# Performance work log

Measured on AMD Instinct MI355X. Metric: run time of the kernel, lower is better.

Reference implementation:

```python
import jax, jax.numpy as jnp
import numpy as np

N, M, D, H, T = 8192, 8192, 64, 32, 8
KERNEL_SCALE = 1.0


def setup_inputs() -> dict:
    key = jax.random.key(0)
    ks = jax.random.split(key, 8)
    s1 = 1.0 / np.sqrt(D)
    s2 = 1.0 / np.sqrt(H)
    return {
        "X": jax.random.normal(ks[0], (N, D), jnp.float32),
        "Y": jax.random.normal(ks[1], (M, D), jnp.float32),
        "Y_target": jax.random.normal(ks[2], (M, T), jnp.float32),
        "W1": jax.random.normal(ks[3], (D, H), jnp.float32) * s1,
        "b1": jnp.zeros((H,), jnp.float32),
        "W2": jax.random.normal(ks[4], (H, H), jnp.float32) * s2,
        "b2": jnp.zeros((H,), jnp.float32),
        "W3": jax.random.normal(ks[5], (H, H), jnp.float32) * s2,
        "b3": jnp.zeros((H,), jnp.float32),
    }


def _mlp(x, W1, b1, W2, b2, W3, b3):
    h = jax.nn.relu(x @ W1 + b1)
    h = jax.nn.relu(h @ W2 + b2)
    return jax.nn.relu(h @ W3 + b3)


def reference(X, Y, Y_target, W1, b1, W2, b2, W3, b3):
    Xf = _mlp(X, W1, b1, W2, b2, W3, b3)  # [N, H]
    Yf = _mlp(Y, W1, b1, W2, b2, W3, b3)  # [M, H]
    sq = (
        jnp.sum(Xf * Xf, axis=1, keepdims=True)
        + jnp.sum(Yf * Yf, axis=1)[None, :]
        - 2.0 * (Xf @ Yf.T)
    )
    sq = jnp.maximum(sq, 0.0)  # guard tiny negatives from cancellation
    kernel = jnp.exp(-sq / (2.0 * KERNEL_SCALE**2))  # [N, M]
    weights = kernel / jnp.sum(kernel, axis=1, keepdims=True)
    return weights @ Y_target  # [N, T]
```

## Files before the change

### kernel.cpp

```cpp
#include <hip/hip_runtime.h>
#include <hip/hip_bf16.h>
#include <cstddef>

#define N_ROWS 8192
#define M_ROWS 8192
#define D_IN   64
#define H_DIM  32
#define T_OUT  8
#define FDIM   48

#define NSPLIT   32
#define JSLICE   (M_ROWS / NSPLIT)
#define JTILE    32
#define NTILES   (JSLICE / JTILE)
#define LOG2E    1.4426950408889634f
#define NHALF_SC (-0.72134752044448169f)

#define KH_OFF 0
#define KL_OFF 3072
#define YH_OFF 6144
#define YL_OFF 8192
#define BUFSZ  10240

typedef _Float16 half8  __attribute__((ext_vector_type(8)));
typedef _Float16 half4v __attribute__((ext_vector_type(4)));
typedef __fp16   fp16x2 __attribute__((ext_vector_type(2)));
typedef float    f32x16 __attribute__((ext_vector_type(16)));

__device__ __forceinline__ half8 ld_h8(const _Float16* p) {
    return *(const half8*)p;
}


__global__ __launch_bounds__(256) void feat_kernel(
    const float* __restrict__ X, const float* __restrict__ Y,
    const float* __restrict__ W1, const float* __restrict__ b1,
    const float* __restrict__ W2, const float* __restrict__ b2,
    const float* __restrict__ W3, const float* __restrict__ b3,
    _Float16* __restrict__ fh, _Float16* __restrict__ fl)
{
    __shared__ float xs [32 * 65];
    __shared__ float w1l[64 * 36];
    __shared__ float w2l[32 * 36];
    __shared__ float w3l[32 * 36];
    __shared__ float h1t[32 * 33];
    __shared__ float h2t[32 * 33];
    __shared__ float psums[8 * 32];
    __shared__ float bl[96];

    const int tid = threadIdx.x;
    const int rowbase = blockIdx.x * 32;
    const bool isX = rowbase < N_ROWS;
    const float* src = isX ? (X + (size_t)rowbase * D_IN)
                           : (Y + (size_t)(rowbase - N_ROWS) * D_IN);

    {
        const float4* g4 = (const float4*)src;
        int i0 = tid * 2;
        float4 v0 = g4[i0], v1 = g4[i0 + 1];
        int f0 = tid * 8;
        int r = f0 >> 6, c = f0 & 63;
        float* dst = xs + r * 65 + c;
        dst[0] = v0.x; dst[1] = v0.y; dst[2] = v0.z; dst[3] = v0.w;
        dst[4] = v1.x; dst[5] = v1.y; dst[6] = v1.z; dst[7] = v1.w;
    }
    {
        const float4* g4 = (const float4*)W1;
        int i0 = tid * 2;
        float4 v0 = g4[i0], v1 = g4[i0 + 1];
        int f0 = tid * 8;
        int r = f0 >> 5, c = f0 & 31;
        float* dst = w1l + r * 36 + c;
        ((float4*)dst)[0] = v0; ((float4*)dst)[1] = v1;
    }
    {
        int f0 = tid * 4;
        int r = f0 >> 5, c = f0 & 31;
        *(float4*)(w2l + r * 36 + c) = ((const float4*)W2)[tid];
        *(float4*)(w3l + r * 36 + c) = ((const float4*)W3)[tid];
    }
    if (tid < 32) { bl[tid] = b1[tid]; bl[32 + tid] = b2[tid]; bl[64 + tid] = b3[tid]; }
    __syncthreads();

    const int r  = tid & 31;
    const int c0 = (tid >> 5) * 4;

    float4 a1 = *(const float4*)(bl + c0);
    #pragma unroll
    for (int k = 0; k < 64; ++k) {
        float xv = xs[r * 65 + k];
        float4 w = *(const float4*)(w1l + k * 36 + c0);
        a1.x = fmaf(xv, w.x, a1.x);
        a1.y = fmaf(xv, w.y, a1.y);
        a1.z = fmaf(xv, w.z, a1.z);
        a1.w = fmaf(xv, w.w, a1.w);
    }
    h1t[(c0 + 0) * 33 + r] = fmaxf(a1.x, 0.f);
    h1t[(c0 + 1) * 33 + r] = fmaxf(a1.y, 0.f);
    h1t[(c0 + 2) * 33 + r] = fmaxf(a1.z, 0.f);
    h1t[(c0 + 3) * 33 + r] = fmaxf(a1.w, 0.f);
    __syncthreads();

    float4 a2 = *(const float4*)(bl + 32 + c0);
    #pragma unroll
    for (int k = 0; k < 32; ++k) {
        float xv = h1t[k * 33 + r];
        float4 w = *(const float4*)(w2l + k * 36 + c0);
        a2.x = fmaf(xv, w.x, a2.x);
        a2.y = fmaf(xv, w.y, a2.y);
        a2.z = fmaf(xv, w.z, a2.z);
        a2.w = fmaf(xv, w.w, a2.w);
    }
    h2t[(c0 + 0) * 33 + r] = fmaxf(a2.x, 0.f);
    h2t[(c0 + 1) * 33 + r] = fmaxf(a2.y, 0.f);
    h2t[(c0 + 2) * 33 + r] = fmaxf(a2.z, 0.f);
    h2t[(c0 + 3) * 33 + r] = fmaxf(a2.w, 0.f);
    __syncthreads();

    float4 a3 = *(const float4*)(bl + 64 + c0);
    #pragma unroll
    for (int k = 0; k < 32; ++k) {
        float xv = h2t[k * 33 + r];
        float4 w = *(const float4*)(w3l + k * 36 + c0);
        a3.x = fmaf(xv, w.x, a3.x);
        a3.y = fmaf(xv, w.y, a3.y);
        a3.z = fmaf(xv, w.z, a3.z);
        a3.w = fmaf(xv, w.w, a3.w);
    }
    float v0 = fmaxf(a3.x, 0.f), v1 = fmaxf(a3.y, 0.f);
    float v2 = fmaxf(a3.z, 0.f), v3 = fmaxf(a3.w, 0.f);

    psums[(tid >> 5) * 32 + r] = v0 * v0 + v1 * v1 + v2 * v2 + v3 * v3;

    const float scale = isX ? LOG2E : 1.0f;
    union { _Float16 h[4]; uint2 u; } hh, ll;
    float sv0 = v0 * scale, sv1 = v1 * scale, sv2 = v2 * scale, sv3 = v3 * scale;
    hh.h[0] = (_Float16)sv0; hh.h[1] = (_Float16)sv1;
    hh.h[2] = (_Float16)sv2; hh.h[3] = (_Float16)sv3;
    ll.h[0] = (_Float16)(sv0 - (float)hh.h[0]);
    ll.h[1] = (_Float16)(sv1 - (float)hh.h[1]);
    ll.h[2] = (_Float16)(sv2 - (float)hh.h[2]);
    ll.h[3] = (_Float16)(sv3 - (float)hh.h[3]);
    {
        const int tile = blockIdx.x;
        const int ch = c0 >> 4, hb = (c0 >> 3) & 1, off = c0 & 7;
        const size_t fi = (((size_t)(tile * 3 + ch) * 64) + hb * 32 + r) * 8 + off;
        *(uint2*)(fh + fi) = hh.u;
        *(uint2*)(fl + fi) = ll.u;
    }

    __syncthreads();
    if (tid < 32) {
        float nrm = 0.f;
        #pragma unroll
        for (int g = 0; g < 8; ++g) nrm += psums[g * 32 + tid];
        float qn = NHALF_SC * nrm;
        float d32 = isX ? qn : 1.0f;
        float d33 = isX ? 1.0f : qn;
        union { _Float16 h[8]; uint4 q; } eh, el, ez;
        #pragma unroll
        for (int i = 0; i < 8; ++i) { eh.h[i] = (_Float16)0.f; el.h[i] = (_Float16)0.f; ez.h[i] = (_Float16)0.f; }
        _Float16 h32 = (_Float16)d32, h33 = (_Float16)d33;
        eh.h[0] = h32; eh.h[1] = h33;
        el.h[0] = (_Float16)(d32 - (float)h32);
        el.h[1] = (_Float16)(d33 - (float)h33);
        const int tile = blockIdx.x;
        const size_t f0 = (((size_t)(tile * 3 + 2) * 64) + tid) * 8;
        const size_t f1 = (((size_t)(tile * 3 + 2) * 64) + 32 + tid) * 8;
        *(uint4*)(fh + f0) = eh.q;  *(uint4*)(fh + f1) = ez.q;
        *(uint4*)(fl + f0) = el.q;  *(uint4*)(fl + f1) = ez.q;
    }
}

__global__ __launch_bounds__(256) void ytt_kernel(
    const float* __restrict__ Yt,
    _Float16* __restrict__ yfh, _Float16* __restrict__ yfl)
{
    const int idx = blockIdx.x * 256 + threadIdx.x;
    const int lane = idx & 63;
    const int jtg  = idx >> 6;
    const int g    = jtg & 3;
    const int jt   = jtg >> 2;
    const int t    = lane & 31;
    const int h    = lane >> 5;
    const int j    = jt * 32 + g * 8 + h * 4;
    union { _Float16 hh[4]; uint2 u; } H, L;
    #pragma unroll
    for (int i = 0; i < 4; ++i) {
        float v = (t < T_OUT) ? Yt[(size_t)(j + i) * T_OUT + t]
                              : (t == 8 ? 1.0f : 0.0f);
        _Float16 hi = (_Float16)v;
        H.hh[i] = hi;
        L.hh[i] = (_Float16)(v - (float)hi);
    }
    *(uint2*)(yfh + (size_t)idx * 4) = H.u;
    *(uint2*)(yfl + (size_t)idx * 4) = L.u;
}

__global__ __launch_bounds__(256, 4) void pair_kernel(
    const _Float16* __restrict__ fh, const _Float16* __restrict__ fl,
    const _Float16* __restrict__ yfh, const _Float16* __restrict__ yfl,
    float* __restrict__ pout, float* __restrict__ psum)
{
    __shared__ char smem[2 * BUFSZ];

    const int tid  = threadIdx.x;
    const int wave = tid >> 6;
    const int lane = tid & 63;
    const int n    = lane & 31;
    const int h    = lane >> 5;

    const int rowtile = blockIdx.x * 4 + wave;
    const int rowbase = rowtile * 32;
    const int s       = blockIdx.y;
    const int ktile0  = (N_ROWS / 32) + s * NTILES;

    const size_t qoff = (size_t)rowtile * 1536 + (size_t)lane * 8;
    half8 qh0 = ld_h8(fh + qoff);
    half8 qh1 = ld_h8(fh + qoff + 512);
    half8 qh2 = ld_h8(fh + qoff + 1024);
    half8 ql0 = ld_h8(fl + qoff);
    half8 ql1 = ld_h8(fl + qoff + 512);
    half8 ql2 = ld_h8(fl + qoff + 1024);

    auto prefetch = [&](int jt, char* buf) {
        const char* srcKh = (const char*)(fh + (size_t)(ktile0 + jt) * 1536);
        const char* srcKl = (const char*)(fl + (size_t)(ktile0 + jt) * 1536);
        const char* srcYh = (const char*)(yfh + (size_t)(s * NTILES + jt) * 1024);
        const char* srcYl = (const char*)(yfl + (size_t)(s * NTILES + jt) * 1024);
        #pragma unroll
        for (int r = 0; r < 3; ++r) {
            const int c0 = wave * 64 + r * 256;
            const int c  = c0 + lane;
            const char* g; char* l;
            if (c0 < 192)      { g = srcKh + (size_t)c * 16;         l = buf + KH_OFF + c * 16; }
            else if (c0 < 384) { g = srcKl + (size_t)(c - 192) * 16; l = buf + KL_OFF + (c - 192) * 16; }
            else if (c0 < 512) { g = srcYh + (size_t)(c - 384) * 16; l = buf + YH_OFF + (c - 384) * 16; }
            else if (c0 < 640) { g = srcYl + (size_t)(c - 512) * 16; l = buf + YL_OFF + (c - 512) * 16; }
            else break;
            __builtin_amdgcn_global_load_lds(
                (const __attribute__((address_space(1))) void*)g,
                (__attribute__((address_space(3))) void*)l, 16, 0, 0);
        }
    };

    f32x16 o = {};

    prefetch(0, smem);
    __syncthreads();

    for (int jt = 0; jt < NTILES; ++jt) {
        char* cur = smem + (jt & 1) * BUFSZ;
        if (jt + 1 < NTILES) prefetch(jt + 1, smem + ((jt + 1) & 1) * BUFSZ);

        half8 kh0 = *(const half8*)(cur + KH_OFF + lane * 16);
        half8 kh1 = *(const half8*)(cur + KH_OFF + 1024 + lane * 16);
        half8 kh2 = *(const half8*)(cur + KH_OFF + 2048 + lane * 16);
        half8 kl0 = *(const half8*)(cur + KL_OFF + lane * 16);
        half8 kl1 = *(const half8*)(cur + KL_OFF + 1024 + lane * 16);
        half8 kl2 = *(const half8*)(cur + KL_OFF + 2048 + lane * 16);

        f32x16 acc = {};
        acc = __builtin_amdgcn_mfma_f32_32x32x16_f16(kh0, qh0, acc, 0, 0, 0);
        acc = __builtin_amdgcn_mfma_f32_32x32x16_f16(kh1, qh1, acc, 0, 0, 0);
        acc = __builtin_amdgcn_mfma_f32_32x32x16_f16(kh2, qh2, acc, 0, 0, 0);
        acc = __builtin_amdgcn_mfma_f32_32x32x16_f16(kh0, ql0, acc, 0, 0, 0);
        acc = __builtin_amdgcn_mfma_f32_32x32x16_f16(kh1, ql1, acc, 0, 0, 0);
        acc = __builtin_amdgcn_mfma_f32_32x32x16_f16(kh2, ql2, acc, 0, 0, 0);
        acc = __builtin_amdgcn_mfma_f32_32x32x16_f16(kl0, qh0, acc, 0, 0, 0);
        acc = __builtin_amdgcn_mfma_f32_32x32x16_f16(kl1, qh1, acc, 0, 0, 0);
        acc = __builtin_amdgcn_mfma_f32_32x32x16_f16(kl2, qh2, acc, 0, 0, 0);

        half4v phi[4];
        #pragma unroll
        for (int g = 0; g < 4; ++g) {
            float w0 = __builtin_amdgcn_exp2f(fminf(acc[4*g+0], 0.f));
            float w1 = __builtin_amdgcn_exp2f(fminf(acc[4*g+1], 0.f));
            float w2 = __builtin_amdgcn_exp2f(fminf(acc[4*g+2], 0.f));
            float w3 = __builtin_amdgcn_exp2f(fminf(acc[4*g+3], 0.f));
            fp16x2 p01 = __builtin_amdgcn_cvt_pkrtz(w0, w1);
            fp16x2 p23 = __builtin_amdgcn_cvt_pkrtz(w2, w3);
            union { unsigned int u[2]; half4v v; } ph;
            ph.u[0] = __builtin_bit_cast(unsigned int, p01);
            ph.u[1] = __builtin_bit_cast(unsigned int, p23);
            phi[g] = ph.v;
        }

        #pragma unroll
        for (int g = 0; g < 4; ++g) {
            half4v bh = *(const half4v*)(cur + YH_OFF + (g * 64 + lane) * 8);
            half4v bv = *(const half4v*)(cur + YL_OFF + (g * 64 + lane) * 8);
            o = __builtin_amdgcn_mfma_f32_32x32x8f16(phi[g], bh, o, 0, 0, 0);
            o = __builtin_amdgcn_mfma_f32_32x32x8f16(phi[g], bv, o, 0, 0, 0);
        }

        __syncthreads();
    }

    const int t = n;
    if (t <= 8) {
        #pragma unroll
        for (int r = 0; r < 16; ++r) {
            int i = (r & 3) + 8 * (r >> 2) + 4 * h;
            int row = rowbase + i;
            float v = o[r];
            if (t < 8)
                pout[((size_t)s * N_ROWS + row) * T_OUT + t] = v;
            else
                psum[(size_t)s * N_ROWS + row] = v;
        }
    }
}

__global__ __launch_bounds__(256) void reduce_kernel(
    const float* __restrict__ pout, const float* __restrict__ psum,
    float* __restrict__ out)
{
    const int id = blockIdx.x * 256 + threadIdx.x;
    const int i = id >> 3;
    float sv = 0.f, sw = 0.f;
    #pragma unroll
    for (int s = 0; s < NSPLIT; ++s) {
        sv += pout[(size_t)s * N_ROWS * T_OUT + id];
        sw += psum[(size_t)s * N_ROWS + i];
    }
    out[id] = sv / sw;
}

extern "C" void kernel_launch(void* const* d_in, const int* in_sizes, int n_in,
                              void* d_out, int out_size, void* d_ws, size_t ws_size,
                              hipStream_t stream)
{
    const float* X  = (const float*)d_in[0];
    const float* Y  = (const float*)d_in[1];
    const float* Yt = (const float*)d_in[2];
    const float* W1 = (const float*)d_in[3];
    const float* b1 = (const float*)d_in[4];
    const float* W2 = (const float*)d_in[5];
    const float* b2 = (const float*)d_in[6];
    const float* W3 = (const float*)d_in[7];
    const float* b3 = (const float*)d_in[8];
    float* out = (float*)d_out;

    char* ws = (char*)d_ws;
    const size_t n_feat = (size_t)((N_ROWS + M_ROWS) / 32) * 3 * 512;
    _Float16* fh  = (_Float16*)ws;   ws += n_feat * 2;
    _Float16* fl  = (_Float16*)ws;   ws += n_feat * 2;
    const size_t n_yf = (size_t)(M_ROWS / JTILE) * 4 * 64 * 4;
    _Float16* yfh = (_Float16*)ws;   ws += n_yf * 2;
    _Float16* yfl = (_Float16*)ws;   ws += n_yf * 2;
    float*    pout = (float*)ws;     ws += (size_t)NSPLIT * N_ROWS * T_OUT * 4;
    float*    psum = (float*)ws;

    feat_kernel<<<(N_ROWS + M_ROWS) / 32, 256, 0, stream>>>(
        X, Y, W1, b1, W2, b2, W3, b3, fh, fl);
    ytt_kernel<<<(M_ROWS / JTILE) * 4 * 64 / 256, 256, 0, stream>>>(Yt, yfh, yfl);

    dim3 grid2(N_ROWS / 128, NSPLIT);
    pair_kernel<<<grid2, 256, 0, stream>>>(fh, fl, yfh, yfl, pout, psum);

    reduce_kernel<<<(N_ROWS * T_OUT) / 256, 256, 0, stream>>>(pout, psum, out);
}
```

Baseline: 112.6 us.

## Merge prep kernels and process two j-tiles per barrier stage

Folds the Y-target conversion into the feature kernel by giving it extra blocks that branch to the conversion path, removing one kernel launch. In the pair kernel, each double-buffer stage now holds two j-tiles and the loop is fully unrolled, so there is one barrier per two tiles instead of one per tile. The deeper prefetch doubles shared memory per block, which may limit how many blocks fit on a CU.

```diff
diff --git a/kernel.cpp b/kernel.cpp
--- a/kernel.cpp
+++ b/kernel.cpp
@@ -21,6 +21,7 @@
 #define YH_OFF 6144
 #define YL_OFF 8192
 #define BUFSZ  10240
+#define STAGESZ (2 * BUFSZ)
 
 typedef _Float16 half8  __attribute__((ext_vector_type(8)));
 typedef _Float16 half4v __attribute__((ext_vector_type(4)));
@@ -32,12 +33,14 @@
 }
 
 
-__global__ __launch_bounds__(256) void feat_kernel(
+__global__ __launch_bounds__(256) void prep_kernel(
     const float* __restrict__ X, const float* __restrict__ Y,
+    const float* __restrict__ Yt,
     const float* __restrict__ W1, const float* __restrict__ b1,
     const float* __restrict__ W2, const float* __restrict__ b2,
     const float* __restrict__ W3, const float* __restrict__ b3,
-    _Float16* __restrict__ fh, _Float16* __restrict__ fl)
+    _Float16* __restrict__ fh, _Float16* __restrict__ fl,
+    _Float16* __restrict__ yfh, _Float16* __restrict__ yfl)
 {
     __shared__ float xs [32 * 65];
     __shared__ float w1l[64 * 36];
@@ -49,6 +52,30 @@
     __shared__ float bl[96];
 
     const int tid = threadIdx.x;
+
+    if (blockIdx.x >= 512) {
+        const int idx = (blockIdx.x - 512) * 256 + tid;
+        const int lane = idx & 63;
+        const int jtg  = idx >> 6;
+        const int g    = jtg & 3;
+        const int jt   = jtg >> 2;
+        const int t    = lane & 31;
+        const int h    = lane >> 5;
+        const int j    = jt * 32 + g * 8 + h * 4;
+        union { _Float16 hh[4]; uint2 u; } H, L;
+        #pragma unroll
+        for (int i = 0; i < 4; ++i) {
+            float v = (t < T_OUT) ? Yt[(size_t)(j + i) * T_OUT + t]
+                                  : (t == 8 ? 1.0f : 0.0f);
+            _Float16 hi = (_Float16)v;
+            H.hh[i] = hi;
+            L.hh[i] = (_Float16)(v - (float)hi);
+        }
+        *(uint2*)(yfh + (size_t)idx * 4) = H.u;
+        *(uint2*)(yfl + (size_t)idx * 4) = L.u;
+        return;
+    }
+
     const int rowbase = blockIdx.x * 32;
     const bool isX = rowbase < N_ROWS;
     const float* src = isX ? (X + (size_t)rowbase * D_IN)
@@ -172,37 +199,12 @@
     }
 }
 
-__global__ __launch_bounds__(256) void ytt_kernel(
-    const float* __restrict__ Yt,
-    _Float16* __restrict__ yfh, _Float16* __restrict__ yfl)
-{
-    const int idx = blockIdx.x * 256 + threadIdx.x;
-    const int lane = idx & 63;
-    const int jtg  = idx >> 6;
-    const int g    = jtg & 3;
-    const int jt   = jtg >> 2;
-    const int t    = lane & 31;
-    const int h    = lane >> 5;
-    const int j    = jt * 32 + g * 8 + h * 4;
-    union { _Float16 hh[4]; uint2 u; } H, L;
-    #pragma unroll
-    for (int i = 0; i < 4; ++i) {
-        float v = (t < T_OUT) ? Yt[(size_t)(j + i) * T_OUT + t]
-                              : (t == 8 ? 1.0f : 0.0f);
-        _Float16 hi = (_Float16)v;
-        H.hh[i] = hi;
-        L.hh[i] = (_Float16)(v - (float)hi);
-    }
-    *(uint2*)(yfh + (size_t)idx * 4) = H.u;
-    *(uint2*)(yfl + (size_t)idx * 4) = L.u;
-}
-
 __global__ __launch_bounds__(256, 4) void pair_kernel(
     const _Float16* __restrict__ fh, const _Float16* __restrict__ fl,
     const _Float16* __restrict__ yfh, const _Float16* __restrict__ yfl,
     float* __restrict__ pout, float* __restrict__ psum)
 {
-    __shared__ char smem[2 * BUFSZ];
+    __shared__ char smem[2 * STAGESZ];
 
     const int tid  = threadIdx.x;
     const int wave = tid >> 6;
@@ -246,13 +248,7 @@
 
     f32x16 o = {};
 
-    prefetch(0, smem);
-    __syncthreads();
-
-    for (int jt = 0; jt < NTILES; ++jt) {
-        char* cur = smem + (jt & 1) * BUFSZ;
-        if (jt + 1 < NTILES) prefetch(jt + 1, smem + ((jt + 1) & 1) * BUFSZ);
-
+    auto compute = [&](const char* cur) {
         half8 kh0 = *(const half8*)(cur + KH_OFF + lane * 16);
         half8 kh1 = *(const half8*)(cur + KH_OFF + 1024 + lane * 16);
         half8 kh2 = *(const half8*)(cur + KH_OFF + 2048 + lane * 16);
@@ -293,7 +289,22 @@
             o = __builtin_amdgcn_mfma_f32_32x32x8f16(phi[g], bh, o, 0, 0, 0);
             o = __builtin_amdgcn_mfma_f32_32x32x8f16(phi[g], bv, o, 0, 0, 0);
         }
-
+    };
+
+    prefetch(0, smem);
+    prefetch(1, smem + BUFSZ);
+    __syncthreads();
+
+    #pragma unroll
+    for (int st = 0; st < NTILES / 2; ++st) {
+        char* cur = smem + (st & 1) * STAGESZ;
+        char* nxt = smem + ((st + 1) & 1) * STAGESZ;
+        if (st + 1 < NTILES / 2) {
+            prefetch(2 * st + 2, nxt);
+            prefetch(2 * st + 3, nxt + BUFSZ);
+        }
+        compute(cur);
+        compute(cur + BUFSZ);
         __syncthreads();
     }
 
@@ -352,9 +363,8 @@
     float*    pout = (float*)ws;     ws += (size_t)NSPLIT * N_ROWS * T_OUT * 4;
     float*    psum = (float*)ws;
 
-    feat_kernel<<<(N_ROWS + M_ROWS) / 32, 256, 0, stream>>>(
-        X, Y, W1, b1, W2, b2, W3, b3, fh, fl);
-    ytt_kernel<<<(M_ROWS / JTILE) * 4 * 64 / 256, 256, 0, stream>>>(Yt, yfh, yfl);
+    prep_kernel<<<512 + 256, 256, 0, stream>>>(
+        X, Y, Yt, W1, b1, W2, b2, W3, b3, fh, fl, yfh, yfl);
 
     dim3 grid2(N_ROWS / 128, NSPLIT);
     pair_kernel<<<grid2, 256, 0, stream>>>(fh, fl, yfh, yfl, pout, psum);
```

New measurement: 111.2 us. Within noise of the previous version (-1.2%).
